# Kernel optimization log

Measured on AMD Instinct MI355X. Metric: run time of the kernel, lower is better.

Reference implementation:

```python
import jax, jax.numpy as jnp
import numpy as np

B, T, E, H = 4, 2048, 1024, 16
D = E // H

def setup_inputs() -> dict:
    key = jax.random.key(0)
    ks = jax.random.split(key, 8)
    s = 0.02
    return {
        "q": jax.random.normal(ks[0], (B, T, E), dtype=jnp.float32),
        "k": jax.random.normal(ks[1], (B, T, E), dtype=jnp.float32),
        "v": jax.random.normal(ks[2], (B, T, E), dtype=jnp.float32),
        "Wq": jax.random.normal(ks[3], (E, E), dtype=jnp.float32) * s,
        "Wk": jax.random.normal(ks[4], (E, E), dtype=jnp.float32) * s,
        "Wv": jax.random.normal(ks[5], (E, E), dtype=jnp.float32) * s,
        "Wp": jax.random.normal(ks[6], (E, E), dtype=jnp.float32) * s,
        "bp": jnp.zeros((E,), dtype=jnp.float32),
    }

def reference(q, k, v, Wq, Wk, Wv, Wp, bp):
    # Linear projections (torch Linear: x @ W.T). NOTE: original code computes
    # key from the already-projected query (k = self.key(q)); external k is unused.
    qp = q @ Wq.T                      # [B,T,E]
    kp = qp @ Wk.T                     # [B,T,E]  <- faithful quirk
    vp = v @ Wv.T                      # [B,T,E]
    qh = qp.reshape(B, T, H, D).transpose(0, 2, 1, 3)  # [B,H,T,D]
    kh = kp.reshape(B, T, H, D).transpose(0, 2, 1, 3)
    vh = vp.reshape(B, T, H, D).transpose(0, 2, 1, 3)
    # Faithful quirk: att = scores / D**(-1/2) == scores * sqrt(D)
    scale = jnp.float32(D) ** 0.5
    att = jnp.einsum('bhtd,bhsd->bhts', qh, kh) * scale  # [B,H,T,T]
    causal = jnp.tril(jnp.ones((T, T), dtype=bool))
    att = jnp.where(causal, att, -jnp.inf)
    att = jax.nn.softmax(att, axis=-1)
    y = jnp.einsum('bhts,bhsd->bhtd', att, vh)           # [B,H,T,D]
    y = y.transpose(0, 2, 1, 3).reshape(B, T, E)
    return y @ Wp.T + bp
```

## Files before the change

kernel.cpp:

```cpp
#include <hip/hip_runtime.h>


typedef unsigned short u16;
typedef unsigned int   u32;
typedef __attribute__((ext_vector_type(8))) __bf16 bf16x8;
typedef __attribute__((ext_vector_type(8))) u16    u16x8;
typedef __attribute__((ext_vector_type(4))) u16    u16x4;
typedef __attribute__((ext_vector_type(4))) float  f32x4;
typedef __attribute__((ext_vector_type(4))) int    i32x4;

#define DEV static __device__ __forceinline__

DEV u16 f2bf(float x){ union{float f;u32 u;}v; v.f=x; u32 r=v.u+0x7fffu+((v.u>>16)&1u); return (u16)(r>>16); }
DEV float bf2f(u16 b){ union{u32 u;float f;}v; v.u=((u32)b)<<16; return v.f; }
DEV f32x4 zero4(){ f32x4 z={0.f,0.f,0.f,0.f}; return z; }
DEV f32x4 mfma16(bf16x8 a, bf16x8 b, f32x4 c){ return __builtin_amdgcn_mfma_f32_16x16x32_bf16(a,b,c,0,0,0); }
DEV void gld16(const u16* g, u16* l){
  __builtin_amdgcn_global_load_lds((const __attribute__((address_space(1))) u32*)g,
                                   (__attribute__((address_space(3))) u32*)l, 16, 0, 0);
}
DEV u32 cvtpk(float lo, float hi){
  u32 r;
  asm("v_cvt_pk_bf16_f32 %0, %1, %2" : "=v"(r) : "v"(lo), "v"(hi));
  return r;
}
DEV float max3(float a, float b, float c){
  float d;
  asm("v_max3_f32 %0, %1, %2, %3" : "=v"(d) : "v"(a), "v"(b), "v"(c));
  return d;
}

constexpr int B_=4, T_=2048, E_=1024;
constexpr int M_=B_*T_;
constexpr float L2E8 = 11.5415603f;

__global__ __launch_bounds__(256)
void cvt_a(const float* __restrict__ q, const float* __restrict__ v,
           u16* __restrict__ qi, u16* __restrict__ vb)
{
  const int j=blockIdx.y;
  const size_t e=((size_t)blockIdx.x*256+threadIdx.x)*8;
  const float* s=(j==0)?q:v;
  f32x4 x0=*reinterpret_cast<const f32x4*>(s+e);
  f32x4 x1=*reinterpret_cast<const f32x4*>(s+e+4);
  u16x8 h,l;
#pragma unroll
  for(int t=0;t<4;t++){
    u16 hh=f2bf(x0[t]); h[t]=hh; l[t]=f2bf(x0[t]-bf2f(hh));
    u16 h2=f2bf(x1[t]); h[t+4]=h2; l[t+4]=f2bf(x1[t]-bf2f(h2));
  }
  if(j==0){
    const size_t row=e>>10, k=e&1023;
    u16* d=qi + row*2048 + (k>>3)*16;
    *reinterpret_cast<u16x8*>(d)=h;
    *reinterpret_cast<u16x8*>(d+8)=l;
  } else {
    *reinterpret_cast<u16x8*>(vb+e)=h;
  }
}

__global__ __launch_bounds__(256)
void cvt_w(const float* __restrict__ Wq, const float* __restrict__ Wk, const float* __restrict__ Wv,
           u16* __restrict__ wqi, u16* __restrict__ wki, u16* __restrict__ wvb)
{
  const int j=blockIdx.y;
  const size_t e=((size_t)blockIdx.x*256+threadIdx.x)*8;
  const float* s=(j==0)?Wq:(j==1)?Wk:Wv;
  f32x4 x0=*reinterpret_cast<const f32x4*>(s+e);
  f32x4 x1=*reinterpret_cast<const f32x4*>(s+e+4);
  u16x8 h,l;
#pragma unroll
  for(int t=0;t<4;t++){
    u16 hh=f2bf(x0[t]); h[t]=hh; l[t]=f2bf(x0[t]-bf2f(hh));
    u16 h2=f2bf(x1[t]); h[t+4]=h2; l[t+4]=f2bf(x1[t]-bf2f(h2));
  }
  if(j==2){ *reinterpret_cast<u16x8*>(wvb+e)=h; return; }
  u16* base=(j==0)?wqi:wki;
  const size_t row=e>>10, k=e&1023;
  u16* d=base + row*2048 + (k>>3)*16;
  *reinterpret_cast<u16x8*>(d)=h;
  *reinterpret_cast<u16x8*>(d+8)=l;
}

__global__ __launch_bounds__(256)
void cvt_p(const float* __restrict__ Wp, u16* __restrict__ wpb)
{
  const size_t e=((size_t)blockIdx.x*256+threadIdx.x)*8;
  f32x4 x0=*reinterpret_cast<const f32x4*>(Wp+e);
  f32x4 x1=*reinterpret_cast<const f32x4*>(Wp+e+4);
  u16x8 h;
#pragma unroll
  for(int t=0;t<4;t++){ h[t]=f2bf(x0[t]); h[t+4]=f2bf(x1[t]); }
  *reinterpret_cast<u16x8*>(wpb+e)=h;
}

template<int SPLIT,int OMODE,int SWAP>
__global__ __launch_bounds__(256)
void gemm(const u16* __restrict__ Ag, const u16* __restrict__ Bg,
          const float* __restrict__ bias,
          u16* __restrict__ Ob, float* __restrict__ Of, int ldc)
{
  __shared__ u16 sA[SPLIT?128*128:128*64];
  __shared__ u16 sB[SPLIT?128*128:128*64];

  const int tid=threadIdx.x, wave=tid>>6, lane=tid&63;
  const int quad=lane>>4, l16=lane&15, sw=l16&7;
  const int wm=(wave>>1)*64, wn=(wave&1)*64;
  const int n0=(SWAP?blockIdx.y:blockIdx.x)*128;
  const int m0=(SWAP?blockIdx.x:blockIdx.y)*128;

  f32x4 acc[4][4];
#pragma unroll
  for(int i=0;i<4;i++)
#pragma unroll
    for(int j=0;j<4;j++) acc[i][j]=zero4();

  for(int k0=0;k0<E_;k0+=64){
    if(SPLIT){
#pragma unroll
      for(int it=0;it<8;it++){
        const int c=it*256+tid, row=c>>4, j=(c&15)^(row&7);
        gld16(Ag + (size_t)(m0+row)*2048 + k0*2 + j*8, &sA[(it*256+wave*64)*8]);
      }
#pragma unroll
      for(int it=0;it<8;it++){
        const int c=it*256+tid, row=c>>4, j=(c&15)^(row&7);
        gld16(Bg + (size_t)(n0+row)*2048 + k0*2 + j*8, &sB[(it*256+wave*64)*8]);
      }
    } else {
#pragma unroll
      for(int it=0;it<4;it++){
        const int c=it*256+tid, row=c>>3, j=(c&7)^(row&7);
        gld16(Ag + (size_t)(m0+row)*1024 + k0 + j*8, &sA[(it*256+wave*64)*8]);
      }
#pragma unroll
      for(int it=0;it<4;it++){
        const int c=it*256+tid, row=c>>3, j=(c&7)^(row&7);
        gld16(Bg + (size_t)(n0+row)*1024 + k0 + j*8, &sB[(it*256+wave*64)*8]);
      }
    }
    __syncthreads();

#pragma unroll
    for(int kk=0;kk<2;kk++){
      if(SPLIT){
        bf16x8 ahh[4],ahl[4],bhh[4],bhl[4];
#pragma unroll
        for(int i=0;i<4;i++){
          const u16* pa=&sA[(wm+i*16+l16)*128];
          const u16* pb=&sB[(wn+i*16+l16)*128];
          const int ch=2*(kk*4+quad);
          ahh[i]=*reinterpret_cast<const bf16x8*>(&pa[((ch  )^sw)*8]);
          ahl[i]=*reinterpret_cast<const bf16x8*>(&pa[((ch+1)^sw)*8]);
          bhh[i]=*reinterpret_cast<const bf16x8*>(&pb[((ch  )^sw)*8]);
          bhl[i]=*reinterpret_cast<const bf16x8*>(&pb[((ch+1)^sw)*8]);
        }
#pragma unroll
        for(int i=0;i<4;i++)
#pragma unroll
          for(int j=0;j<4;j++){
            acc[i][j]=mfma16(ahh[i],bhh[j],acc[i][j]);
            acc[i][j]=mfma16(ahh[i],bhl[j],acc[i][j]);
            acc[i][j]=mfma16(ahl[i],bhh[j],acc[i][j]);
          }
      } else {
        bf16x8 a[4],b[4];
#pragma unroll
        for(int i=0;i<4;i++){
          a[i]=*reinterpret_cast<const bf16x8*>(&sA[(wm+i*16+l16)*64 + (((kk*4+quad)^sw)*8)]);
          b[i]=*reinterpret_cast<const bf16x8*>(&sB[(wn+i*16+l16)*64 + (((kk*4+quad)^sw)*8)]);
        }
#pragma unroll
        for(int i=0;i<4;i++)
#pragma unroll
          for(int j=0;j<4;j++)
            acc[i][j]=mfma16(a[i],b[j],acc[i][j]);
      }
    }
    __syncthreads();
  }

#pragma unroll
  for(int i=0;i<4;i++)
#pragma unroll
    for(int j=0;j<4;j++){
      const int col=n0+wn+j*16+l16;
#pragma unroll
      for(int r=0;r<4;r++){
        const int row=m0+wm+i*16+quad*4+r;
        float v=acc[i][j][r];
        if(OMODE==2)      Of[(size_t)row*ldc+col]=v+bias[col];
        else if(OMODE==1) Ob[(size_t)row*ldc+col]=f2bf(v);
        else {
          u16 hh=f2bf(v);
          const size_t base=(size_t)row*2048 + (size_t)(col>>3)*16 + (col&7);
          Ob[base]=hh; Ob[base+8]=f2bf(v-bf2f(hh));
        }
      }
    }
}

__global__ __launch_bounds__(256)
void attn(const u16* __restrict__ qpi, const u16* __restrict__ kpi,
          const u16* __restrict__ vpT, u16* __restrict__ yout)
{
  __shared__ u16 sK [2][64*128];
  __shared__ u16 sVT[2][64*64];

  const int tid=threadIdx.x, wave=tid>>6, lane=tid&63;
  const int quad=lane>>4, l16=lane&15, sw=l16&7;
  const int qt=15-((int)blockIdx.x>>6);
  const int bh=blockIdx.x&63;
  const int b=bh>>4, h=bh&15;
  const int qr0=qt*128+wave*32;

  const f32x4 FZ=zero4();
  bf16x8 ONES;
  {
    u16x8 o={0x3f80,0x3f80,0x3f80,0x3f80,0x3f80,0x3f80,0x3f80,0x3f80};
    ONES=*reinterpret_cast<bf16x8*>(&o);
  }

  auto STAGE=[&](int buf, int kt2){
    const int s0=kt2*64;
#pragma unroll
    for(int it=0;it<4;it++){
      const int c=it*256+tid, row=c>>4, j=(c&15)^(row&7);
      gld16(kpi + (size_t)(b*T_+s0+row)*2048 + h*128 + j*8,
            &sK[buf][(it*256+wave*64)*8]);
    }
#pragma unroll
    for(int it=0;it<2;it++){
      const int c=it*256+tid, row=c>>3, j=(c&7)^(row&7);
      gld16(vpT + (size_t)(h*64+row)*8192 + b*T_ + s0 + j*8,
            &sVT[buf][(it*256+wave*64)*8]);
    }
  };

  bf16x8 qfh[2][2], qfl[2][2];
#pragma unroll
  for(int mt=0;mt<2;mt++)
#pragma unroll
    for(int ksv=0;ksv<2;ksv++){
      const size_t off=(size_t)(b*T_+qr0+mt*16+l16)*2048 + h*128 + (ksv*4+quad)*16;
      qfh[mt][ksv]=*reinterpret_cast<const bf16x8*>(qpi+off);
      qfl[mt][ksv]=*reinterpret_cast<const bf16x8*>(qpi+off+8);
    }

  float mst[2]={-1e30f,-1e30f};
  f32x4 lacc[2]={FZ,FZ};
  f32x4 oacc[2][4];
#pragma unroll
  for(int mt=0;mt<2;mt++)
#pragma unroll
    for(int dt=0;dt<4;dt++) oacc[mt][dt]=zero4();

  const int nkt=2*(qt+1);
  STAGE(0, 0);
  __syncthreads();

  for(int kt=0;kt<nkt;kt++){
    const int cur=kt&1;
    if(kt+1<nkt) STAGE(cur^1, kt+1);
    const int s0=kt*64;

    if(s0<=qr0+31){
      f32x4 sacc[4][2];
      __builtin_amdgcn_s_setprio(1);
#pragma unroll
      for(int st=0;st<4;st++)
#pragma unroll
        for(int ksv=0;ksv<2;ksv++){
          const u16* pk=&sK[cur][(st*16+l16)*128];
          const int ch=2*(ksv*4+quad);
          bf16x8 kh=*reinterpret_cast<const bf16x8*>(&pk[((ch  )^sw)*8]);
          bf16x8 kl=*reinterpret_cast<const bf16x8*>(&pk[((ch+1)^sw)*8]);
#pragma unroll
          for(int mt=0;mt<2;mt++){
            sacc[st][mt]=mfma16(kh,qfh[mt][ksv], (ksv==0)?FZ:sacc[st][mt]);
            sacc[st][mt]=mfma16(kl,qfh[mt][ksv],sacc[st][mt]);
            sacc[st][mt]=mfma16(kh,qfl[mt][ksv],sacc[st][mt]);
          }
        }
      __builtin_amdgcn_s_setprio(0);
      const bool needmask=(s0+63>qr0);
      u32 pk_[4][2][2];
#pragma unroll
      for(int mt=0;mt<2;mt++){
        const int qrow=qr0+mt*16+l16;
        float v_[16];
#pragma unroll
        for(int st=0;st<4;st++)
#pragma unroll
          for(int r=0;r<4;r++){
            float v=sacc[st][mt][r];
            if(needmask && (s0+st*16+quad*4+r>qrow)) v=-1e30f;
            sacc[st][mt][r]=v;
            v_[st*4+r]=v;
          }
        float m0=max3(v_[0],v_[1],v_[2]);
        float m1=max3(v_[3],v_[4],v_[5]);
        float m2=max3(v_[6],v_[7],v_[8]);
        float m3=max3(v_[9],v_[10],v_[11]);
        float m4=max3(v_[12],v_[13],v_[14]);
        float mloc=fmaxf(max3(m0,m1,m2), max3(m3,m4,v_[15]));
        mloc=fmaxf(mloc,__shfl_xor(mloc,16,64));
        mloc=fmaxf(mloc,__shfl_xor(mloc,32,64));
        float cexp;
        if(__all(mloc <= mst[mt]+1.0f)){
          cexp=mst[mt]*L2E8;
        } else {
          const float nm=fmaxf(mst[mt],mloc);
          const float alpha=exp2f((mst[mt]-nm)*L2E8);
          mst[mt]=nm;
          lacc[mt]*=alpha;
#pragma unroll
          for(int dt=0;dt<4;dt++) oacc[mt][dt]*=alpha;
          cexp=nm*L2E8;
        }
#pragma unroll
        for(int st=0;st<4;st++){
#pragma unroll
          for(int r=0;r<4;r++){
            float p=exp2f(__builtin_fmaf(sacc[st][mt][r],L2E8,-cexp));
            sacc[st][mt][r]=p;
          }
          pk_[st][mt][0]=cvtpk(sacc[st][mt][0],sacc[st][mt][1]);
          pk_[st][mt][1]=cvtpk(sacc[st][mt][2],sacc[st][mt][3]);
        }
      }
      const int srcA=(2*(quad&1))*16+l16, srcB=srcA+16;
      const bool hs=(quad>=2);
#pragma unroll
      for(int ksv=0;ksv<2;ksv++){
        bf16x8 b2[2];
#pragma unroll
        for(int mt=0;mt<2;mt++){
          int e0=__shfl((int)pk_[2*ksv  ][mt][0],srcA,64);
          int g0=__shfl((int)pk_[2*ksv+1][mt][0],srcA,64);
          int e1=__shfl((int)pk_[2*ksv  ][mt][1],srcA,64);
          int g1=__shfl((int)pk_[2*ksv+1][mt][1],srcA,64);
          int e2=__shfl((int)pk_[2*ksv  ][mt][0],srcB,64);
          int g2=__shfl((int)pk_[2*ksv+1][mt][0],srcB,64);
          int e3=__shfl((int)pk_[2*ksv  ][mt][1],srcB,64);
          int g3=__shfl((int)pk_[2*ksv+1][mt][1],srcB,64);
          i32x4 bd={ hs?g0:e0, hs?g1:e1, hs?g2:e2, hs?g3:e3 };
          b2[mt]=*reinterpret_cast<bf16x8*>(&bd);
        }
        __builtin_amdgcn_s_setprio(1);
        lacc[0]=mfma16(ONES,b2[0],lacc[0]);
        lacc[1]=mfma16(ONES,b2[1],lacc[1]);
#pragma unroll
        for(int dt=0;dt<4;dt++){
          bf16x8 va=*reinterpret_cast<const bf16x8*>(&sVT[cur][(dt*16+l16)*64 + (((ksv*4+quad)^sw)*8)]);
#pragma unroll
          for(int mt=0;mt<2;mt++)
            oacc[mt][dt]=mfma16(va,b2[mt],oacc[mt][dt]);
        }
        __builtin_amdgcn_s_setprio(0);
      }
    }
    __syncthreads();
  }

#pragma unroll
  for(int mt=0;mt<2;mt++){
    const float inv=1.0f/lacc[mt][0];
    const size_t rb=(size_t)(b*T_+qr0+mt*16+l16)*1024 + h*64;
#pragma unroll
    for(int dt=0;dt<4;dt++){
      u16x4 o4;
#pragma unroll
      for(int r=0;r<4;r++) o4[r]=f2bf(oacc[mt][dt][r]*inv);
      *reinterpret_cast<u16x4*>(yout + rb + dt*16 + quad*4)=o4;
    }
  }
}

extern "C" void kernel_launch(void* const* d_in, const int* in_sizes, int n_in,
                              void* d_out, int out_size, void* d_ws, size_t ws_size,
                              hipStream_t stream)
{
  const float* q =(const float*)d_in[0];
  const float* v =(const float*)d_in[2];
  const float* Wq=(const float*)d_in[3];
  const float* Wk=(const float*)d_in[4];
  const float* Wv=(const float*)d_in[5];
  const float* Wp=(const float*)d_in[6];
  const float* bp=(const float*)d_in[7];
  float* out=(float*)d_out;

  const size_t NE=(size_t)M_*E_;
  const size_t WE=(size_t)E_*E_;
  u16* wsv=(u16*)d_ws;
  u16* qsl_i=wsv;
  u16* qp_i =wsv+2*NE;
  u16* kp_i =wsv;
  u16* wp_b =wsv+2*NE;
  u16* vpT  =wsv+4*NE;
  u16* ybf  =wsv+5*NE;
  u16* og   =(u16*)d_out;
  u16* wq_i =og;
  u16* wk_i =og+2*WE;
  u16* wv_b =og+4*WE;
  u16* vb   =og+5*WE;

  dim3 blk(256);
  cvt_a<<<dim3(NE/2048,2), blk, 0, stream>>>(q, v, qsl_i, vb);
  cvt_w<<<dim3(WE/2048,3), blk, 0, stream>>>(Wq, Wk, Wv, wq_i, wk_i, wv_b);

  dim3 gs(M_/128, E_/128);
  gemm<1,0,1><<<gs, blk, 0, stream>>>(qsl_i, wq_i, nullptr, qp_i, nullptr, 0);
  gemm<1,0,1><<<gs, blk, 0, stream>>>(qp_i, wk_i, nullptr, kp_i, nullptr, 0);
  gemm<0,1,0><<<dim3(M_/128, E_/128), blk, 0, stream>>>(wv_b, vb, nullptr, vpT, nullptr, M_);
  attn<<<dim3(1024), blk, 0, stream>>>(qp_i, kp_i, vpT, ybf);
  cvt_p<<<dim3(WE/2048), blk, 0, stream>>>(Wp, wp_b);
  gemm<0,2,1><<<gs, blk, 0, stream>>>(ybf, wp_b, bp, nullptr, out, E_);
}
```

Baseline: 419.3 us.

## Merge K and V projection GEMMs into one launch and halve split-GEMM LDS

The K projection (split bf16 hi/lo) and the V projection GEMMs are merged into a single 1024-block kernel that branches on block index, so the two independent GEMMs share one launch and can fill the GPU together. The split-precision GEMM path now steps K by 32 instead of 64, which halves its shared-memory tile to 32 KB. That gives a uniform LDS footprint and more resident blocks per CU, at the cost of twice as many barrier and load iterations. The GEMM body is factored into a device function that both kernels reuse.

```diff
diff --git a/kernel.cpp b/kernel.cpp
--- a/kernel.cpp
+++ b/kernel.cpp
@@ -94,20 +94,15 @@
   *reinterpret_cast<u16x8*>(wpb+e)=h;
 }
 
-template<int SPLIT,int OMODE,int SWAP>
-__global__ __launch_bounds__(256)
-void gemm(const u16* __restrict__ Ag, const u16* __restrict__ Bg,
-          const float* __restrict__ bias,
-          u16* __restrict__ Ob, float* __restrict__ Of, int ldc)
-{
-  __shared__ u16 sA[SPLIT?128*128:128*64];
-  __shared__ u16 sB[SPLIT?128*128:128*64];
-
+template<int SPLIT,int OMODE>
+DEV void gemm_body(u16* sA, u16* sB, int m0, int n0,
+                   const u16* __restrict__ Ag, const u16* __restrict__ Bg,
+                   const float* __restrict__ bias,
+                   u16* __restrict__ Ob, float* __restrict__ Of, int ldc)
+{
   const int tid=threadIdx.x, wave=tid>>6, lane=tid&63;
   const int quad=lane>>4, l16=lane&15, sw=l16&7;
   const int wm=(wave>>1)*64, wn=(wave&1)*64;
-  const int n0=(SWAP?blockIdx.y:blockIdx.x)*128;
-  const int m0=(SWAP?blockIdx.x:blockIdx.y)*128;
 
   f32x4 acc[4][4];
 #pragma unroll
@@ -115,19 +110,44 @@
 #pragma unroll
     for(int j=0;j<4;j++) acc[i][j]=zero4();
 
-  for(int k0=0;k0<E_;k0+=64){
-    if(SPLIT){
-#pragma unroll
-      for(int it=0;it<8;it++){
-        const int c=it*256+tid, row=c>>4, j=(c&15)^(row&7);
+  if(SPLIT){
+    for(int k0=0;k0<E_;k0+=32){
+#pragma unroll
+      for(int it=0;it<4;it++){
+        const int c=it*256+tid, row=c>>3, j=(c&7)^(row&7);
         gld16(Ag + (size_t)(m0+row)*2048 + k0*2 + j*8, &sA[(it*256+wave*64)*8]);
       }
 #pragma unroll
-      for(int it=0;it<8;it++){
-        const int c=it*256+tid, row=c>>4, j=(c&15)^(row&7);
+      for(int it=0;it<4;it++){
+        const int c=it*256+tid, row=c>>3, j=(c&7)^(row&7);
         gld16(Bg + (size_t)(n0+row)*2048 + k0*2 + j*8, &sB[(it*256+wave*64)*8]);
       }
-    } else {
+      __syncthreads();
+
+      const int ch=2*quad;
+      bf16x8 bhh[4],bhl[4];
+#pragma unroll
+      for(int j=0;j<4;j++){
+        const u16* pb=&sB[(wn+j*16+l16)*64];
+        bhh[j]=*reinterpret_cast<const bf16x8*>(&pb[((ch  )^sw)*8]);
+        bhl[j]=*reinterpret_cast<const bf16x8*>(&pb[((ch+1)^sw)*8]);
+      }
+#pragma unroll
+      for(int i=0;i<4;i++){
+        const u16* pa=&sA[(wm+i*16+l16)*64];
+        bf16x8 ahh=*reinterpret_cast<const bf16x8*>(&pa[((ch  )^sw)*8]);
+        bf16x8 ahl=*reinterpret_cast<const bf16x8*>(&pa[((ch+1)^sw)*8]);
+#pragma unroll
+        for(int j=0;j<4;j++){
+          acc[i][j]=mfma16(ahh,bhh[j],acc[i][j]);
+          acc[i][j]=mfma16(ahh,bhl[j],acc[i][j]);
+          acc[i][j]=mfma16(ahl,bhh[j],acc[i][j]);
+        }
+      }
+      __syncthreads();
+    }
+  } else {
+    for(int k0=0;k0<E_;k0+=64){
 #pragma unroll
       for(int it=0;it<4;it++){
         const int c=it*256+tid, row=c>>3, j=(c&7)^(row&7);
@@ -138,32 +158,10 @@
         const int c=it*256+tid, row=c>>3, j=(c&7)^(row&7);
         gld16(Bg + (size_t)(n0+row)*1024 + k0 + j*8, &sB[(it*256+wave*64)*8]);
       }
-    }
-    __syncthreads();
-
-#pragma unroll
-    for(int kk=0;kk<2;kk++){
-      if(SPLIT){
-        bf16x8 ahh[4],ahl[4],bhh[4],bhl[4];
-#pragma unroll
-        for(int i=0;i<4;i++){
-          const u16* pa=&sA[(wm+i*16+l16)*128];
-          const u16* pb=&sB[(wn+i*16+l16)*128];
-          const int ch=2*(kk*4+quad);
-          ahh[i]=*reinterpret_cast<const bf16x8*>(&pa[((ch  )^sw)*8]);
-          ahl[i]=*reinterpret_cast<const bf16x8*>(&pa[((ch+1)^sw)*8]);
-          bhh[i]=*reinterpret_cast<const bf16x8*>(&pb[((ch  )^sw)*8]);
-          bhl[i]=*reinterpret_cast<const bf16x8*>(&pb[((ch+1)^sw)*8]);
-        }
-#pragma unroll
-        for(int i=0;i<4;i++)
-#pragma unroll
-          for(int j=0;j<4;j++){
-            acc[i][j]=mfma16(ahh[i],bhh[j],acc[i][j]);
-            acc[i][j]=mfma16(ahh[i],bhl[j],acc[i][j]);
-            acc[i][j]=mfma16(ahl[i],bhh[j],acc[i][j]);
-          }
-      } else {
+      __syncthreads();
+
+#pragma unroll
+      for(int kk=0;kk<2;kk++){
         bf16x8 a[4],b[4];
 #pragma unroll
         for(int i=0;i<4;i++){
@@ -176,8 +174,8 @@
           for(int j=0;j<4;j++)
             acc[i][j]=mfma16(a[i],b[j],acc[i][j]);
       }
-    }
-    __syncthreads();
+      __syncthreads();
+    }
   }
 
 #pragma unroll
@@ -198,6 +196,36 @@
         }
       }
     }
+}
+
+template<int SPLIT,int OMODE,int SWAP>
+__global__ __launch_bounds__(256)
+void gemm(const u16* __restrict__ Ag, const u16* __restrict__ Bg,
+          const float* __restrict__ bias,
+          u16* __restrict__ Ob, float* __restrict__ Of, int ldc)
+{
+  __shared__ u16 smem[2*128*64];
+  const int n0=(SWAP?blockIdx.y:blockIdx.x)*128;
+  const int m0=(SWAP?blockIdx.x:blockIdx.y)*128;
+  gemm_body<SPLIT,OMODE>(smem, smem+128*64, m0, n0, Ag, Bg, bias, Ob, Of, ldc);
+}
+
+__global__ __launch_bounds__(256)
+void gemm_kv(const u16* __restrict__ qp_i, const u16* __restrict__ wk_i,
+             u16* __restrict__ kp_i,
+             const u16* __restrict__ wv_b, const u16* __restrict__ vb,
+             u16* __restrict__ vpT)
+{
+  __shared__ u16 smem[2*128*64];
+  const int bid=(int)blockIdx.x;
+  if(bid<512){
+    const int m0=(bid&63)*128, n0=(bid>>6)*128;
+    gemm_body<1,0>(smem, smem+128*64, m0, n0, qp_i, wk_i, nullptr, kp_i, nullptr, 0);
+  } else {
+    const int b2=bid-512;
+    const int n0=(b2&63)*128, m0=(b2>>6)*128;
+    gemm_body<0,1>(smem, smem+128*64, m0, n0, wv_b, vb, nullptr, vpT, nullptr, M_);
+  }
 }
 
 __global__ __launch_bounds__(256)
@@ -411,8 +439,7 @@
 
   dim3 gs(M_/128, E_/128);
   gemm<1,0,1><<<gs, blk, 0, stream>>>(qsl_i, wq_i, nullptr, qp_i, nullptr, 0);
-  gemm<1,0,1><<<gs, blk, 0, stream>>>(qp_i, wk_i, nullptr, kp_i, nullptr, 0);
-  gemm<0,1,0><<<dim3(M_/128, E_/128), blk, 0, stream>>>(wv_b, vb, nullptr, vpT, nullptr, M_);
+  gemm_kv<<<dim3(1024), blk, 0, stream>>>(qp_i, wk_i, kp_i, wv_b, vb, vpT);
   attn<<<dim3(1024), blk, 0, stream>>>(qp_i, kp_i, vpT, ybf);
   cvt_p<<<dim3(WE/2048), blk, 0, stream>>>(Wp, wp_b);
   gemm<0,2,1><<<gs, blk, 0, stream>>>(ybf, wp_b, bp, nullptr, out, E_);
```

After: 435.1 us. 3.8% more time.
